# Optimization experiments

Hardware: AMD Instinct MI355X
Metric: run time of the kernel (lower is better)

## Reference

```python
import jax, jax.numpy as jnp
import numpy as np

B, L, A = 256, 512, 40          # proteins, residues per protein, atoms per drug
FD, FT, LD = 78, 54, 128        # drug feat, protein feat, latent dim
P = L + 1                       # residues + 1 appended drug super-node


def setup_inputs() -> dict:
    key = jax.random.key(0)
    ks = iter(jax.random.split(key, 48))
    Nd = B * A
    # drug graphs: chain bonds, both directions
    i = np.arange(A - 1)
    s = np.concatenate([i, i + 1]); d = np.concatenate([i + 1, i])
    off = (np.arange(B) * A)[:, None]
    drug_ei = jnp.asarray(np.stack([(s[None] + off).ravel(), (d[None] + off).ravel()]), jnp.int32)
    drug_batch = jnp.asarray(np.repeat(np.arange(B), A), jnp.int32)
    # protein graphs: residue chain + drug super-node (local idx L) connected to all residues in order
    r = np.arange(L - 1)
    ps = np.concatenate([r, r + 1, np.full(L, L), np.arange(L)])
    pd = np.concatenate([r + 1, r, np.arange(L), np.full(L, L)])
    poff = (np.arange(B) * P)[:, None]
    prot_ei = jnp.asarray(np.stack([(ps[None] + poff).ravel(), (pd[None] + poff).ravel()]), jnp.int32)
    prot_batch = jnp.asarray(np.repeat(np.arange(B), P), jnp.int32)
    E2 = B * (2 * (L - 1) + 2 * L)

    def lin(fi, fo):
        return jax.random.normal(next(ks), (fi, fo), jnp.float32) / np.float32(np.sqrt(fi))

    def vec(fo):
        return jnp.zeros((fo,), jnp.float32)

    return dict(
        drug_x=jax.random.normal(next(ks), (Nd, FD), jnp.float32),
        drug_ei=drug_ei, drug_batch=drug_batch,
        prot_x=jax.random.normal(next(ks), (B * P, FT), jnp.float32),
        prot_ei=prot_ei, prot_batch=prot_batch,
        prot_ea=jax.random.uniform(next(ks), (E2,), jnp.float32),
        W_c1d=lin(FD, FD), b_c1d=vec(FD),
        W_c2d=lin(FD, 2 * FD), b_c2d=vec(2 * FD),
        W_rd_g=lin(2 * FD, 2 * FD), b_rd_g=vec(2 * FD), W_rd_l=lin(2 * FD, 2 * FD),
        W_fg1d=lin(2 * FD, 1024), b_fg1d=vec(1024),
        W_fg2d=lin(1024, FT), b_fg2d=vec(FT),
        W_fg3d=lin(FT, 2 * LD), b_fg3d=vec(2 * LD),
        W_att1=lin(FT, FT), b_att1=vec(FT),
        W_att2=lin(FT, 1), b_att2=vec(1),
        W_c1t=lin(FT, LD), b_c1t=vec(LD),
        W_c2t=lin(LD, 2 * LD), b_c2t=vec(2 * LD),
        W_rt_g=lin(2 * LD, 2 * LD), b_rt_g=vec(2 * LD), W_rt_l=lin(2 * LD, 2 * LD),
        W_fg1t=lin(2 * LD, 1024), b_fg1t=vec(1024),
        W_fg2t=lin(1024, 2 * LD), b_fg2t=vec(2 * LD),
        W_fc1=lin(4 * LD, 1024), b_fc1=vec(1024),
        W_fc2=lin(1024, 512), b_fc2=vec(512),
        W_out=lin(512, 1), b_out=vec(1),
    )


def _gcn(x, W, b, src, dst, ew, n):
    # PyG GCNConv: symmetric norm with self-loops (fill value 1), optional edge weights
    h = x @ W
    deg = jax.ops.segment_sum(ew, dst, num_segments=n) + 1.0
    dinv = jax.lax.rsqrt(deg)
    norm = dinv[src] * ew * dinv[dst]
    agg = jax.ops.segment_sum(h[src] * norm[:, None], dst, num_segments=n)
    return agg + h * (dinv * dinv)[:, None] + b


def _rblock(x, Wg, bg, Wl, src, dst, ew, n):
    h = jax.nn.relu(_gcn(x, Wg, bg, src, dst, ew, n))
    return jax.nn.relu(h @ Wl + x)


def reference(drug_x, drug_ei, drug_batch, prot_x, prot_ei, prot_batch, prot_ea,
              W_c1d, b_c1d, W_c2d, b_c2d, W_rd_g, b_rd_g, W_rd_l,
              W_fg1d, b_fg1d, W_fg2d, b_fg2d, W_fg3d, b_fg3d,
              W_att1, b_att1, W_att2, b_att2,
              W_c1t, b_c1t, W_c2t, b_c2t, W_rt_g, b_rt_g, W_rt_l,
              W_fg1t, b_fg1t, W_fg2t, b_fg2t,
              W_fc1, b_fc1, W_fc2, b_fc2, W_out, b_out):
    relu = jax.nn.relu
    Nd, N2 = drug_x.shape[0], prot_x.shape[0]
    sd, dd = drug_ei[0], drug_ei[1]
    ewd = jnp.ones(sd.shape[0], drug_x.dtype)
    x = relu(_gcn(drug_x, W_c1d, b_c1d, sd, dd, ewd, Nd))
    x = relu(_gcn(x, W_c2d, b_c2d, sd, dd, ewd, Nd))
    for _ in range(4):  # shared-weight residual block applied num_rblock times
        x = _rblock(x, W_rd_g, b_rd_g, W_rd_l, sd, dd, ewd, Nd)
    xg = jax.ops.segment_max(x, drug_batch, num_segments=B)  # global max pool
    x = relu(xg @ W_fg1d + b_fg1d)
    x = x @ W_fg2d + b_fg2d                                   # [B, FT]
    x_chg = relu(x @ W_fg3d + b_fg3d)                          # [B, 2*LD]
    # vectorized per-protein attention (replaces the python loop over prot_lens)
    res = prot_x.reshape(B, P, FT)[:, :L]                      # residues only
    att = jnp.tanh(res @ W_att1 + b_att1) @ W_att2 + b_att2    # [B, L, 1]
    att = jax.nn.softmax(att[..., 0], axis=1)                  # [B, L]
    att_node = jnp.concatenate([att, jnp.zeros((B, 1), att.dtype)], 1).reshape(-1)
    drug_idx = (jnp.arange(B) + 1) * P - 1
    is_drug = jnp.zeros((N2,), bool).at[drug_idx].set(True)
    st, dt = prot_ei[0], prot_ei[1]
    # edges touching a drug super-node get that residue's attention weight
    ea = jnp.where(is_drug[st], att_node[dt], jnp.where(is_drug[dt], att_node[st], prot_ea))
    x2 = prot_x.at[drug_idx].set(x)                            # inject drug embeddings
    x2 = relu(_gcn(x2, W_c1t, b_c1t, st, dt, ea, N2))
    x2 = relu(_gcn(x2, W_c2t, b_c2t, st, dt, ea, N2))
    ew1 = jnp.ones(st.shape[0], x2.dtype)
    for _ in range(4):
        x2 = _rblock(x2, W_rt_g, b_rt_g, W_rt_l, st, dt, ew1, N2)
    x2r = x2.reshape(B, P, 2 * LD)
    x2g = x2r[:, :L].max(axis=1)                               # gmp over residues (drug node masked out)
    drug_after = x2r[:, L]
    x2v = relu(x2g @ W_fg1t + b_fg1t) @ W_fg2t + b_fg2t
    xm = jnp.maximum(drug_after, x_chg)                        # max_pool1d(kernel=2) over the pair
    xc = jnp.concatenate([xm, x2v], 1)
    xc = relu(xc @ W_fc1 + b_fc1)
    xc = relu(xc @ W_fc2 + b_fc2)
    return xc @ W_out + b_out
```

## Files before the change

kernel.cpp:

```cpp
#include <hip/hip_runtime.h>
#include <cstdio>

#define B_   256
#define L_   512
#define A_   40
#define FD_  78
#define FT_  54
#define LD_  128
#define P_   513
#define ND_  (B_*A_)
#define N2_  (B_*P_)
#define EB_  2046

typedef __attribute__((ext_vector_type(8))) short short8;
typedef __attribute__((ext_vector_type(4))) float floatx4;
typedef unsigned short u16;

__device__ __forceinline__ short f2bf(float f) {
    union { float f; unsigned u; } v; v.f = f;
    unsigned u = v.u;
    u += 0x7fff + ((u >> 16) & 1);
    return (short)(u >> 16);
}
__device__ __forceinline__ float bf2f(u16 s) {
    union { unsigned u; float f; } v; v.u = ((unsigned)s) << 16; return v.f;
}

#define TBK 32
#define LDK 40

__global__ __launch_bounds__(256) void gemm_mfma_k(
    const float* __restrict__ A, const short* __restrict__ WT,
    float* __restrict__ C, int M, int N, int K, int Kp)
{
    __shared__ short As[128 * LDK];
    __shared__ short Bs[128 * LDK];
    const int bm = blockIdx.y * 128;
    const int bn = blockIdx.x * 128;
    const int tid  = threadIdx.x;
    const int wave = tid >> 6, lane = tid & 63;
    const int wm = (wave >> 1) * 64, wn = (wave & 1) * 64;
    const int lrow = lane & 15, quad = lane >> 4;

    floatx4 acc[4][4] = {};

    for (int k0 = 0; k0 < Kp; k0 += TBK) {
#pragma unroll
        for (int it = 0; it < 2; ++it) {
            int g   = it * 256 + tid;
            int row = g >> 2, kg = g & 3;
            int kb  = k0 + kg * 8;
            const float* arow = A + (size_t)(bm + row) * K + kb;
            short8 av;
#pragma unroll
            for (int j = 0; j < 8; ++j) av[j] = (kb + j < K) ? f2bf(arow[j]) : (short)0;
            *(short8*)&As[row * LDK + kg * 8] = av;
            *(short8*)&Bs[row * LDK + kg * 8] = *(const short8*)(WT + (size_t)(bn + row) * Kp + kb);
        }
        __syncthreads();
        short8 af[4], bfv[4];
#pragma unroll
        for (int i = 0; i < 4; ++i)
            af[i] = *(short8*)&As[(wm + i * 16 + lrow) * LDK + quad * 8];
#pragma unroll
        for (int j = 0; j < 4; ++j)
            bfv[j] = *(short8*)&Bs[(wn + j * 16 + lrow) * LDK + quad * 8];
#pragma unroll
        for (int i = 0; i < 4; ++i)
#pragma unroll
            for (int j = 0; j < 4; ++j)
                acc[i][j] = __builtin_amdgcn_mfma_f32_16x16x32_bf16(af[i], bfv[j], acc[i][j], 0, 0, 0);
        __syncthreads();
    }
#pragma unroll
    for (int i = 0; i < 4; ++i) {
        int grow0 = bm + wm + i * 16 + quad * 4;
#pragma unroll
        for (int j = 0; j < 4; ++j) {
            int col = bn + wn + j * 16 + lrow;
            size_t base = (size_t)grow0 * N + col;
#pragma unroll
            for (int r = 0; r < 4; ++r)
                C[base + (size_t)r * N] = acc[i][j][r];
        }
    }
}

__global__ __launch_bounds__(256) void gemm_bb_k(
    const u16* __restrict__ A, int lda, const short* __restrict__ WT, int Kp,
    const u16* __restrict__ resid, u16* __restrict__ C, int N, int act)
{
    __shared__ short As[128 * LDK];
    __shared__ short Bs[128 * LDK];
    const int bm = blockIdx.y * 128;
    const int bn = blockIdx.x * 128;
    const int tid  = threadIdx.x;
    const int wave = tid >> 6, lane = tid & 63;
    const int wm = (wave >> 1) * 64, wn = (wave & 1) * 64;
    const int lrow = lane & 15, quad = lane >> 4;

    floatx4 acc[4][4] = {};

    for (int k0 = 0; k0 < Kp; k0 += TBK) {
#pragma unroll
        for (int it = 0; it < 2; ++it) {
            int g   = it * 256 + tid;
            int row = g >> 2, kg = g & 3;
            int kb  = k0 + kg * 8;
            *(short8*)&As[row * LDK + kg * 8] = *(const short8*)(A + (size_t)(bm + row) * lda + kb);
            *(short8*)&Bs[row * LDK + kg * 8] = *(const short8*)(WT + (size_t)(bn + row) * Kp + kb);
        }
        __syncthreads();
        short8 af[4], bfv[4];
#pragma unroll
        for (int i = 0; i < 4; ++i)
            af[i] = *(short8*)&As[(wm + i * 16 + lrow) * LDK + quad * 8];
#pragma unroll
        for (int j = 0; j < 4; ++j)
            bfv[j] = *(short8*)&Bs[(wn + j * 16 + lrow) * LDK + quad * 8];
#pragma unroll
        for (int i = 0; i < 4; ++i)
#pragma unroll
            for (int j = 0; j < 4; ++j)
                acc[i][j] = __builtin_amdgcn_mfma_f32_16x16x32_bf16(af[i], bfv[j], acc[i][j], 0, 0, 0);
        __syncthreads();
    }
#pragma unroll
    for (int i = 0; i < 4; ++i) {
        int grow0 = bm + wm + i * 16 + quad * 4;
#pragma unroll
        for (int j = 0; j < 4; ++j) {
            int col = bn + wn + j * 16 + lrow;
            size_t base = (size_t)grow0 * N + col;
#pragma unroll
            for (int r = 0; r < 4; ++r) {
                float v = acc[i][j][r];
                size_t idx = base + (size_t)r * N;
                if (resid) v += bf2f(resid[idx]);
                if (act)   v = fmaxf(v, 0.f);
                C[idx] = (u16)f2bf(v);
            }
        }
    }
}

template<int KT>
__global__ __launch_bounds__(256, 3) void gemm_n256pw_k(
    const u16* __restrict__ A, const short* __restrict__ WT,
    const u16* __restrict__ resid, u16* __restrict__ C, int act,
    const float* __restrict__ cInF, float* __restrict__ Wacc)
{
    constexpr int K = KT * TBK;
    __shared__ short As[64 * LDK];
    __shared__ short Bs[256 * LDK];
    const int bm = blockIdx.x * 64;
    const int tid  = threadIdx.x;
    const int wave = tid >> 6, lane = tid & 63;
    const int wn = wave * 64;
    const int lrow = lane & 15, quad = lane >> 4;
    const int srow = tid >> 2, skg = tid & 3;

    floatx4 acc[4][4] = {};

    short8 aR[KT];
#pragma unroll
    for (int kt = 0; kt < KT; ++kt)
        aR[kt] = *(const short8*)(A + (size_t)(bm + srow) * K + kt * TBK + skg * 8);
    short8 bReg[4];
#pragma unroll
    for (int it = 0; it < 4; ++it)
        bReg[it] = *(const short8*)(WT + (size_t)(it * 64 + srow) * K + skg * 8);

#pragma unroll
    for (int kt = 0; kt < KT; ++kt) {
        *(short8*)&As[srow * LDK + skg * 8] = aR[kt];
#pragma unroll
        for (int it = 0; it < 4; ++it)
            *(short8*)&Bs[(it * 64 + srow) * LDK + skg * 8] = bReg[it];
        __syncthreads();
        if (kt + 1 < KT) {
            int kn = (kt + 1) * TBK;
#pragma unroll
            for (int it = 0; it < 4; ++it)
                bReg[it] = *(const short8*)(WT + (size_t)(it * 64 + srow) * K + kn + skg * 8);
        }
        short8 af[4], bfv[4];
#pragma unroll
        for (int i = 0; i < 4; ++i)
            af[i] = *(short8*)&As[(i * 16 + lrow) * LDK + quad * 8];
#pragma unroll
        for (int j = 0; j < 4; ++j)
            bfv[j] = *(short8*)&Bs[(wn + j * 16 + lrow) * LDK + quad * 8];
#pragma unroll
        for (int i = 0; i < 4; ++i)
#pragma unroll
            for (int j = 0; j < 4; ++j)
                acc[i][j] = __builtin_amdgcn_mfma_f32_16x16x32_bf16(af[i], bfv[j], acc[i][j], 0, 0, 0);
        __syncthreads();
    }
#pragma unroll
    for (int i = 0; i < 4; ++i) {
        int grow0 = bm + i * 16 + quad * 4;
#pragma unroll
        for (int j = 0; j < 4; ++j) {
            int col = wn + j * 16 + lrow;
            size_t base = (size_t)grow0 * 256 + col;
#pragma unroll
            for (int r = 0; r < 4; ++r) {
                float v = acc[i][j][r];
                size_t idx = base + (size_t)r * 256;
                if (resid) v += bf2f(resid[idx]);
                if (act)   v = fmaxf(v, 0.f);
                C[idx] = (u16)f2bf(v);
            }
        }
    }
    if (cInF) {
        const int b0 = bm / P_;
        const int b1 = (bm + 63) / P_;
        float s0[4] = {0.f, 0.f, 0.f, 0.f};
        float s1[4] = {0.f, 0.f, 0.f, 0.f};
#pragma unroll
        for (int i = 0; i < 4; ++i) {
#pragma unroll
            for (int r = 0; r < 4; ++r) {
                int grow = bm + i * 16 + quad * 4 + r;
                float ci = cInF[grow];
                bool hi = (grow / P_) != b0;
#pragma unroll
                for (int j = 0; j < 4; ++j) {
                    float v = ci * acc[i][j][r];
                    if (hi) s1[j] += v; else s0[j] += v;
                }
            }
        }
#pragma unroll
        for (int j = 0; j < 4; ++j) {
            s0[j] += __shfl_xor(s0[j], 16);
            s0[j] += __shfl_xor(s0[j], 32);
            s1[j] += __shfl_xor(s1[j], 16);
            s1[j] += __shfl_xor(s1[j], 32);
        }
        if (quad == 0) {
#pragma unroll
            for (int j = 0; j < 4; ++j) {
                int col = wn + j * 16 + lrow;
                atomicAdd(&Wacc[(size_t)b0 * 256 + col], s0[j]);
                if (b1 != b0) atomicAdd(&Wacc[(size_t)b1 * 256 + col], s1[j]);
            }
        }
    }
}

template<int KT>
__global__ __launch_bounds__(256, 3) void gemm_aggl_k(
    const u16* __restrict__ U, const short* __restrict__ WT,
    const float* __restrict__ cPc, const float* __restrict__ cNc,
    const float* __restrict__ cDc, const float* __restrict__ cSc,
    const float* __restrict__ Wacc, const float* __restrict__ bias,
    const u16* __restrict__ resid, u16* __restrict__ C)
{
    constexpr int K = KT * TBK;
    __shared__ short As[64 * LDK];
    __shared__ short Bs[256 * LDK];
    const int bm = blockIdx.x * 64;
    const int tid  = threadIdx.x;
    const int wave = tid >> 6, lane = tid & 63;
    const int wn = wave * 64;
    const int lrow = lane & 15, quad = lane >> 4;
    const int srow = tid >> 2, skg = tid & 3;

    const int r    = bm + srow;
    const int bl   = r / P_;
    const int irow = r - bl * P_;
    const bool isD = (irow == L_);
    const size_t rD = (size_t)bl * P_ + L_;
    const int rm = (r == 0) ? 0 : r - 1;
    const int rp = (r == N2_ - 1) ? r : r + 1;
    const float cs = cSc[r];
    const float cp = isD ? 0.f : cPc[r];
    const float cn = isD ? 0.f : cNc[r];
    const float cd = isD ? 0.f : cDc[r];
    const float* wrow = Wacc + (size_t)bl * 256;

    floatx4 acc[4][4] = {};

    const u16* uSp = U + (size_t)r  * K + skg * 8;
    const u16* uMp = U + (size_t)rm * K + skg * 8;
    const u16* uPp = U + (size_t)rp * K + skg * 8;
    const u16* uDp = U + (size_t)rD * K + skg * 8;

    short8 uS[KT];
#pragma unroll
    for (int kt = 0; kt < KT; ++kt) uS[kt] = *(const short8*)(uSp + kt * TBK);
    short8 uM = *(const short8*)uMp;
    short8 uP = *(const short8*)uPp;
    short8 uD = *(const short8*)uDp;
    short8 bReg[4];
#pragma unroll
    for (int it = 0; it < 4; ++it)
        bReg[it] = *(const short8*)(WT + (size_t)(it * 64 + srow) * K + skg * 8);

#pragma unroll
    for (int kt = 0; kt < KT; ++kt) {
        const int kb = kt * TBK + skg * 8;
        float4 bi0 = *(const float4*)(bias + kb);
        float4 bi1 = *(const float4*)(bias + kb + 4);
        float bv[8] = {bi0.x, bi0.y, bi0.z, bi0.w, bi1.x, bi1.y, bi1.z, bi1.w};
        if (isD) {
            float4 w0 = *(const float4*)(wrow + kb);
            float4 w1 = *(const float4*)(wrow + kb + 4);
            bv[0] += w0.x; bv[1] += w0.y; bv[2] += w0.z; bv[3] += w0.w;
            bv[4] += w1.x; bv[5] += w1.y; bv[6] += w1.z; bv[7] += w1.w;
        }
        short8 av;
#pragma unroll
        for (int e = 0; e < 8; ++e) {
            float v = cs * bf2f((u16)uS[kt][e]) + cp * bf2f((u16)uM[e])
                    + cn * bf2f((u16)uP[e]) + cd * bf2f((u16)uD[e]) + bv[e];
            av[e] = f2bf(fmaxf(v, 0.f));
        }
        *(short8*)&As[srow * LDK + skg * 8] = av;
#pragma unroll
        for (int it = 0; it < 4; ++it)
            *(short8*)&Bs[(it * 64 + srow) * LDK + skg * 8] = bReg[it];
        __syncthreads();
        if (kt + 1 < KT) {
            const int kn = (kt + 1) * TBK;
            uM = *(const short8*)(uMp + kn);
            uP = *(const short8*)(uPp + kn);
            uD = *(const short8*)(uDp + kn);
#pragma unroll
            for (int it = 0; it < 4; ++it)
                bReg[it] = *(const short8*)(WT + (size_t)(it * 64 + srow) * K + kn + skg * 8);
        }
        short8 af[4], bfv[4];
#pragma unroll
        for (int i = 0; i < 4; ++i)
            af[i] = *(short8*)&As[(i * 16 + lrow) * LDK + quad * 8];
#pragma unroll
        for (int j = 0; j < 4; ++j)
            bfv[j] = *(short8*)&Bs[(wn + j * 16 + lrow) * LDK + quad * 8];
#pragma unroll
        for (int i = 0; i < 4; ++i)
#pragma unroll
            for (int j = 0; j < 4; ++j)
                acc[i][j] = __builtin_amdgcn_mfma_f32_16x16x32_bf16(af[i], bfv[j], acc[i][j], 0, 0, 0);
        __syncthreads();
    }
#pragma unroll
    for (int i = 0; i < 4; ++i) {
        int grow0 = bm + i * 16 + quad * 4;
#pragma unroll
        for (int j = 0; j < 4; ++j) {
            int col = wn + j * 16 + lrow;
            size_t base = (size_t)grow0 * 256 + col;
#pragma unroll
            for (int r2 = 0; r2 < 4; ++r2) {
                float v = acc[i][j][r2];
                size_t idx = base + (size_t)r2 * 256;
                v += bf2f(resid[idx]);
                v = fmaxf(v, 0.f);
                C[idx] = (u16)f2bf(v);
            }
        }
    }
}

static inline void gemm_n256(const u16* A, int K, const short* WT,
                             const u16* resid, u16* C, int act,
                             const float* cInF, float* Wacc, hipStream_t s)
{
    dim3 g(N2_ / 64), b(256);
    if (K == 128)
        hipLaunchKernelGGL((gemm_n256pw_k<4>), g, b, 0, s, A, WT, resid, C, act, cInF, Wacc);
    else
        hipLaunchKernelGGL((gemm_n256pw_k<8>), g, b, 0, s, A, WT, resid, C, act, cInF, Wacc);
}

__global__ void wt_cvt_k(const float* __restrict__ W, short* __restrict__ WT,
                         int K, int Nreal, int Kp, int Ntot)
{
    int idx = blockIdx.x * 256 + threadIdx.x;
    if (idx >= Ntot * Kp) return;
    int n = idx / Kp, k = idx - n * Kp;
    WT[idx] = (k < K && n < Nreal) ? f2bf(W[(size_t)k * Nreal + n]) : (short)0;
}

#define BM 64
#define BN 64
#define BKK 16
__global__ __launch_bounds__(256) void gemm_k(
    const float* __restrict__ Amat, const float* __restrict__ Wmat,
    const float* __restrict__ bias, const float* __restrict__ resid,
    float* __restrict__ Cmat, int M, int N, int K, int act)
{
    __shared__ float As[BKK][BM + 4];
    __shared__ float Ws[BKK][BN];
    const int bm = blockIdx.y * BM;
    const int bn = blockIdx.x * BN;
    const int tx = threadIdx.x, ty = threadIdx.y;
    const int tid = ty * 16 + tx;
    float acc[4][4] = {};

    for (int k0 = 0; k0 < K; k0 += BKK) {
#pragma unroll
        for (int j = 0; j < 4; ++j) {
            int l = tid + 256 * j;
            int m = l >> 4, kk = l & 15;
            int gm = bm + m, gk = k0 + kk;
            As[kk][m] = (gm < M && gk < K) ? Amat[(size_t)gm * K + gk] : 0.f;
        }
#pragma unroll
        for (int j = 0; j < 4; ++j) {
            int l = tid + 256 * j;
            int kk = l >> 6, n = l & 63;
            int gk = k0 + kk, gn = bn + n;
            Ws[kk][n] = (gk < K && gn < N) ? Wmat[(size_t)gk * N + gn] : 0.f;
        }
        __syncthreads();
#pragma unroll
        for (int k = 0; k < BKK; ++k) {
            float4 a4 = *(const float4*)&As[k][ty * 4];
            float4 w4 = *(const float4*)&Ws[k][tx * 4];
            float av[4] = {a4.x, a4.y, a4.z, a4.w};
            float wv[4] = {w4.x, w4.y, w4.z, w4.w};
#pragma unroll
            for (int i = 0; i < 4; ++i)
#pragma unroll
                for (int j = 0; j < 4; ++j)
                    acc[i][j] = fmaf(av[i], wv[j], acc[i][j]);
        }
        __syncthreads();
    }
#pragma unroll
    for (int i = 0; i < 4; ++i) {
        int gm = bm + ty * 4 + i;
        if (gm >= M) continue;
#pragma unroll
        for (int j = 0; j < 4; ++j) {
            int gn = bn + tx * 4 + j;
            if (gn >= N) continue;
            float v = acc[i][j];
            if (bias)  v += bias[gn];
            if (resid) v += resid[(size_t)gm * N + gn];
            if (act)   v = fmaxf(v, 0.f);
            Cmat[(size_t)gm * N + gn] = v;
        }
    }
}

static inline void gemm(const float* A, const float* W, const float* bias,
                        const float* resid, float* C, int M, int N, int K, int act,
                        hipStream_t s)
{
    dim3 g((N + BN - 1) / BN, (M + BM - 1) / BM), b(16, 16);
    hipLaunchKernelGGL(gemm_k, g, b, 0, s, A, W, bias, resid, C, M, N, K, act);
}

__global__ __launch_bounds__(256) void gemm_skA_k(
    const float* __restrict__ Amat, const float* __restrict__ Wmat,
    float* __restrict__ part, int M, int N, int K, int Kc)
{
    __shared__ float As[BKK][BM + 4];
    __shared__ float Ws[BKK][BN];
    const int bm = blockIdx.y * BM;
    const int bn = blockIdx.x * BN;
    const int sk = blockIdx.z;
    const int kb0  = sk * Kc;
    const int kend = min(K, kb0 + Kc);
    const int tx = threadIdx.x, ty = threadIdx.y;
    const int tid = ty * 16 + tx;
    float acc[4][4] = {};

    for (int k0 = kb0; k0 < kend; k0 += BKK) {
#pragma unroll
        for (int j = 0; j < 4; ++j) {
            int l = tid + 256 * j;
            int m = l >> 4, kk = l & 15;
            int gm = bm + m, gk = k0 + kk;
            As[kk][m] = (gm < M && gk < kend) ? Amat[(size_t)gm * K + gk] : 0.f;
        }
#pragma unroll
        for (int j = 0; j < 4; ++j) {
            int l = tid + 256 * j;
            int kk = l >> 6, n = l & 63;
            int gk = k0 + kk, gn = bn + n;
            Ws[kk][n] = (gk < kend && gn < N) ? Wmat[(size_t)gk * N + gn] : 0.f;
        }
        __syncthreads();
#pragma unroll
        for (int k = 0; k < BKK; ++k) {
            float4 a4 = *(const float4*)&As[k][ty * 4];
            float4 w4 = *(const float4*)&Ws[k][tx * 4];
            float av[4] = {a4.x, a4.y, a4.z, a4.w};
            float wv[4] = {w4.x, w4.y, w4.z, w4.w};
#pragma unroll
            for (int i = 0; i < 4; ++i)
#pragma unroll
                for (int j = 0; j < 4; ++j)
                    acc[i][j] = fmaf(av[i], wv[j], acc[i][j]);
        }
        __syncthreads();
    }
#pragma unroll
    for (int i = 0; i < 4; ++i) {
        int gm = bm + ty * 4 + i;
        if (gm >= M) continue;
#pragma unroll
        for (int j = 0; j < 4; ++j) {
            int gn = bn + tx * 4 + j;
            if (gn >= N) continue;
            part[((size_t)sk * M + gm) * N + gn] = acc[i][j];
        }
    }
}

__global__ void gemm_skB_k(const float* __restrict__ part, const float* __restrict__ bias,
                           float* __restrict__ C, int M, int N, int SK, int act)
{
    int idx = blockIdx.x * 256 + threadIdx.x;
    if (idx >= M * N) return;
    int n = idx % N;
    float v = bias ? bias[n] : 0.f;
    for (int s = 0; s < SK; ++s) v += part[(size_t)s * M * N + idx];
    if (act) v = fmaxf(v, 0.f);
    C[idx] = v;
}

static inline void gemm_sk(const float* A, const float* W, const float* bias,
                           float* C, float* skbuf, int M, int N, int K, int SK, int act,
                           hipStream_t s)
{
    int Kc = (K + SK - 1) / SK;
    dim3 g((N + 63) / 64, (M + 63) / 64, SK), b(16, 16);
    hipLaunchKernelGGL(gemm_skA_k, g, b, 0, s, A, W, skbuf, M, N, K, Kc);
    hipLaunchKernelGGL(gemm_skB_k, dim3((M * N + 255) / 256), dim3(256), 0, s,
                       skbuf, bias, C, M, N, SK, act);
}

__global__ void drug_agg_k(const float* __restrict__ h, const float* __restrict__ bias,
                           float* __restrict__ out, int F)
{
    int r = blockIdx.x;
    int a = r % A_;
    int t = threadIdx.x;
    if (t >= F) return;
    const float DI2 = 0.70710678118654752f;
    const float DI3 = 0.57735026918962576f;
    float da = (a == 0 || a == A_ - 1) ? DI2 : DI3;
    const float* hs = h + (size_t)r * F;
    float v = da * da * hs[t] + bias[t];
    if (a > 0) {
        float dp = (a - 1 == 0) ? DI2 : DI3;
        v += dp * da * hs[t - F];
    }
    if (a < A_ - 1) {
        float dn = (a + 1 == A_ - 1) ? DI2 : DI3;
        v += dn * da * hs[t + F];
    }
    out[(size_t)r * F + t] = fmaxf(v, 0.f);
}

__global__ void drug_max_k(const float* __restrict__ x, float* __restrict__ xg)
{
    int b = blockIdx.x, t = threadIdx.x;
    if (t >= 2 * FD_) return;
    const float* xb = x + (size_t)b * A_ * (2 * FD_);
    float m = -INFINITY;
    for (int a = 0; a < A_; ++a) m = fmaxf(m, xb[a * (2 * FD_) + t]);
    xg[b * (2 * FD_) + t] = m;
}

__global__ __launch_bounds__(256) void att_dot_k(
    const float* __restrict__ Hs, const float* __restrict__ b1,
    const float* __restrict__ W2, const float* __restrict__ b2,
    float* __restrict__ scores)
{
    int w = threadIdx.x >> 6, lane = threadIdx.x & 63;
    float b1v = (lane < FT_) ? b1[lane] : 0.f;
    float w2v = (lane < FT_) ? W2[lane] : 0.f;
    float b2v = b2[0];
    int base = blockIdx.x * 64 + w * 16;
    for (int rr = 0; rr < 16; ++rr) {
        int r = base + rr;
        float v = 0.f;
        if (lane < FT_) v = tanhf(Hs[(size_t)r * 128 + lane] + b1v) * w2v;
#pragma unroll
        for (int o = 32; o; o >>= 1) v += __shfl_down(v, o);
        if (lane == 0) {
            int bl = r / P_, i = r - bl * P_;
            if (i < L_) scores[bl * L_ + i] = v + b2v;
        }
    }
}

__global__ __launch_bounds__(512) void softmax_k(
    const float* __restrict__ scores, float* __restrict__ att, float* __restrict__ attsum)
{
    int b = blockIdx.x, t = threadIdx.x;
    __shared__ float sm[8];
    __shared__ float bcast;
    float v = scores[b * L_ + t];
    float m = v;
#pragma unroll
    for (int o = 32; o; o >>= 1) m = fmaxf(m, __shfl_down(m, o));
    if ((t & 63) == 0) sm[t >> 6] = m;
    __syncthreads();
    if (t == 0) { float mm = sm[0]; for (int i = 1; i < 8; ++i) mm = fmaxf(mm, sm[i]); bcast = mm; }
    __syncthreads();
    float mx = bcast;
    float e = expf(v - mx);
    float s = e;
#pragma unroll
    for (int o = 32; o; o >>= 1) s += __shfl_down(s, o);
    __syncthreads();
    if ((t & 63) == 0) sm[t >> 6] = s;
    __syncthreads();
    if (t == 0) { float ss = 0; for (int i = 0; i < 8; ++i) ss += sm[i]; bcast = ss; }
    __syncthreads();
    float a = e / bcast;
    att[b * L_ + t] = a;
    float s2 = a;
#pragma unroll
    for (int o = 32; o; o >>= 1) s2 += __shfl_down(s2, o);
    __syncthreads();
    if ((t & 63) == 0) sm[t >> 6] = s2;
    __syncthreads();
    if (t == 0) { float ss = 0; for (int i = 0; i < 8; ++i) ss += sm[i]; attsum[b] = ss; }
}

__global__ void coef_deg_k(const float* __restrict__ prot_ea, const float* __restrict__ att,
                           const float* __restrict__ attsum, float* __restrict__ dinv, int use_ea)
{
    int r = blockIdx.x * 256 + threadIdx.x;
    if (r >= N2_) return;
    int b = r / P_, i = r - b * P_;
    float deg;
    if (i == L_) {
        deg = 1.f + (use_ea ? attsum[b] : (float)L_);
    } else {
        float wP = (i >= 1)      ? (use_ea ? prot_ea[b * EB_ + (i - 1)]   : 1.f) : 0.f;
        float wN = (i <= L_ - 2) ? (use_ea ? prot_ea[b * EB_ + 511 + i]   : 1.f) : 0.f;
        float wD = use_ea ? att[b * L_ + i] : 1.f;
        deg = 1.f + wP + wN + wD;
    }
    dinv[r] = rsqrtf(deg);
}

__global__ void coef_k(const float* __restrict__ dinv, const float* __restrict__ prot_ea,
                       const float* __restrict__ att, float* __restrict__ cP, float* __restrict__ cN,
                       float* __restrict__ cD, float* __restrict__ cS, float* __restrict__ cIn,
                       float* __restrict__ cInF, int use_ea)
{
    int r = blockIdx.x * 256 + threadIdx.x;
    if (r >= N2_) return;
    int b = r / P_, i = r - b * P_;
    float di = dinv[r];
    cS[r] = di * di;
    if (i == L_) { cP[r] = 0.f; cN[r] = 0.f; cD[r] = 0.f; cInF[r] = 0.f; return; }
    float wP = (i >= 1)      ? (use_ea ? prot_ea[b * EB_ + (i - 1)] : 1.f) : 0.f;
    float wN = (i <= L_ - 2) ? (use_ea ? prot_ea[b * EB_ + 511 + i] : 1.f) : 0.f;
    float wD = use_ea ? att[b * L_ + i] : 1.f;
    float dD = dinv[b * P_ + L_];
    cP[r] = (i >= 1)      ? dinv[r - 1] * wP * di : 0.f;
    cN[r] = (i <= L_ - 2) ? dinv[r + 1] * wN * di : 0.f;
    cD[r] = dD * wD * di;
    float ci = di * wD * dD;
    cIn[b * L_ + i] = ci;
    cInF[r] = ci;
}

template<int F>
__global__ __launch_bounds__(256) void prot_agg_res_k(
    const u16* __restrict__ h, const float* __restrict__ cP,
    const float* __restrict__ cN, const float* __restrict__ cD,
    const float* __restrict__ cS, const float* __restrict__ cIn,
    const float* __restrict__ bias, u16* __restrict__ outp,
    float* __restrict__ Wacc)
{
    constexpr int G = F / 8;
    constexpr int RPB = 256 / G;
    __shared__ float pacc[RPB * F];
    int t = threadIdx.x;
    int rl = t / G, g = t - rl * G;
    int base = blockIdx.x * RPB;
    int r = base + rl;
    int bl = r / P_, i = r - bl * P_;
    int f0 = g * 8;
    const u16* hs = h + (size_t)r * F + f0;
    if (i == L_) {
#pragma unroll
        for (int e = 0; e < 8; ++e) pacc[rl * F + f0 + e] = 0.f;
    } else {
        const u16* hd = h + ((size_t)bl * P_ + L_) * F + f0;
        float cs = cS[r], cd = cD[r], cp = cP[r], cn = cN[r];
        float ci = cIn[bl * L_ + i];
        short8 vs = *(const short8*)hs;
        short8 vd = *(const short8*)hd;
        short8 vp = *(const short8*)(hs - (i > 0 ? F : 0));
        short8 vn = *(const short8*)(hs + F);
        short8 ov;
#pragma unroll
        for (int e = 0; e < 8; ++e) {
            float hv = bf2f((u16)vs[e]);
            pacc[rl * F + f0 + e] = ci * hv;
            float v = cs * hv + cd * bf2f((u16)vd[e]) + bias[f0 + e];
            v += cp * bf2f((u16)vp[e]);
            v += cn * bf2f((u16)vn[e]);
            ov[e] = f2bf(fmaxf(v, 0.f));
        }
        *(short8*)(outp + (size_t)r * F + f0) = ov;
    }
    __syncthreads();
    int f = t;
    if (f < F) {
        int b0   = base / P_;
        int bend = (base + RPB - 1) / P_;
        float s0 = 0.f, s1 = 0.f;
#pragma unroll
        for (int rr = 0; rr < RPB; ++rr) {
            float v = pacc[rr * F + f];
            if ((base + rr) / P_ == b0) s0 += v; else s1 += v;
        }
        atomicAdd(&Wacc[(size_t)b0 * F + f], s0);
        if (bend != b0) atomicAdd(&Wacc[(size_t)bend * F + f], s1);
    }
}

__global__ void drug_fin_k(const float* __restrict__ Wacc, const u16* __restrict__ h,
                           const float* __restrict__ cS, const float* __restrict__ bias,
                           u16* __restrict__ outp, int F)
{
    int bl = blockIdx.x, t = threadIdx.x;
    if (t >= F) return;
    size_t rD = (size_t)bl * P_ + L_;
    float v = Wacc[(size_t)bl * F + t] + cS[rD] * bf2f(h[rD * F + t]) + bias[t];
    outp[rD * F + t] = (u16)f2bf(fmaxf(v, 0.f));
}

__global__ void xin_k(const float* __restrict__ prot_x, const float* __restrict__ t2d,
                      u16* __restrict__ Xin)
{
    int idx = blockIdx.x * 256 + threadIdx.x;
    if (idx >= N2_ * 64) return;
    int r = idx >> 6, t = idx & 63;
    int bl = r / P_, i = r - bl * P_;
    float v = 0.f;
    if (t < FT_) v = (i == L_) ? t2d[bl * FT_ + t] : prot_x[(size_t)r * FT_ + t];
    Xin[idx] = (u16)f2bf(v);
}

__global__ __launch_bounds__(256) void x2g_bf2_k(const u16* __restrict__ X,
                                                 float* __restrict__ x2g, float* __restrict__ da)
{
    __shared__ float red[2048];
    int t = threadIdx.x;
    int rl = t >> 5, g = t & 31;
    int bl = blockIdx.x, f0 = g * 8;
    const u16* xb = X + (size_t)bl * P_ * 256;
    float m[8];
#pragma unroll
    for (int e = 0; e < 8; ++e) m[e] = -INFINITY;
    for (int j = rl; j < L_; j += 8) {
        short8 v = *(const short8*)(xb + (size_t)j * 256 + f0);
#pragma unroll
        for (int e = 0; e < 8; ++e) m[e] = fmaxf(m[e], bf2f((u16)v[e]));
    }
#pragma unroll
    for (int e = 0; e < 8; ++e) red[rl * 256 + f0 + e] = m[e];
    __syncthreads();
    if (rl == 0) {
        short8 vd = *(const short8*)(xb + (size_t)L_ * 256 + f0);
#pragma unroll
        for (int e = 0; e < 8; ++e) {
            float v = red[f0 + e];
            for (int rr = 1; rr < 8; ++rr) v = fmaxf(v, red[rr * 256 + f0 + e]);
            x2g[bl * 256 + f0 + e] = v;
            da[bl * 256 + f0 + e] = bf2f((u16)vd[e]);
        }
    }
}

__global__ void build_xc_k(const float* __restrict__ da, const float* __restrict__ x_chg,
                           const float* __restrict__ x2v, float* __restrict__ xc)
{
    int idx = blockIdx.x * 256 + threadIdx.x;
    if (idx >= B_ * 512) return;
    int b = idx >> 9, c = idx & 511;
    float v = (c < 256) ? fmaxf(da[b * 256 + c], x_chg[b * 256 + c])
                        : x2v[b * 256 + (c - 256)];
    xc[idx] = v;
}

__global__ __launch_bounds__(64) void out_k(const float* __restrict__ f2,
                                            const float* __restrict__ W,
                                            const float* __restrict__ bias,
                                            float* __restrict__ out)
{
    int row = blockIdx.x, t = threadIdx.x;
    float v = 0.f;
    for (int k = t; k < 512; k += 64) v = fmaf(f2[(size_t)row * 512 + k], W[k], v);
#pragma unroll
    for (int o = 32; o; o >>= 1) v += __shfl_down(v, o);
    if (t == 0) out[row] = v + bias[0];
}

extern "C" void kernel_launch(void* const* d_in, const int* in_sizes, int n_in,
                              void* d_out, int out_size, void* d_ws, size_t ws_size,
                              hipStream_t stream)
{
    const float* drug_x  = (const float*)d_in[0];
    const float* prot_x  = (const float*)d_in[3];
    const float* prot_ea = (const float*)d_in[6];
    const float* W_c1d = (const float*)d_in[7];   const float* b_c1d = (const float*)d_in[8];
    const float* W_c2d = (const float*)d_in[9];   const float* b_c2d = (const float*)d_in[10];
    const float* W_rd_g = (const float*)d_in[11]; const float* b_rd_g = (const float*)d_in[12];
    const float* W_rd_l = (const float*)d_in[13];
    const float* W_fg1d = (const float*)d_in[14]; const float* b_fg1d = (const float*)d_in[15];
    const float* W_fg2d = (const float*)d_in[16]; const float* b_fg2d = (const float*)d_in[17];
    const float* W_fg3d = (const float*)d_in[18]; const float* b_fg3d = (const float*)d_in[19];
    const float* W_att1 = (const float*)d_in[20]; const float* b_att1 = (const float*)d_in[21];
    const float* W_att2 = (const float*)d_in[22]; const float* b_att2 = (const float*)d_in[23];
    const float* W_c1t = (const float*)d_in[24];  const float* b_c1t = (const float*)d_in[25];
    const float* W_c2t = (const float*)d_in[26];  const float* b_c2t = (const float*)d_in[27];
    const float* W_rt_g = (const float*)d_in[28]; const float* b_rt_g = (const float*)d_in[29];
    const float* W_rt_l = (const float*)d_in[30];
    const float* W_fg1t = (const float*)d_in[31]; const float* b_fg1t = (const float*)d_in[32];
    const float* W_fg2t = (const float*)d_in[33]; const float* b_fg2t = (const float*)d_in[34];
    const float* W_fc1 = (const float*)d_in[35];  const float* b_fc1 = (const float*)d_in[36];
    const float* W_fc2 = (const float*)d_in[37];  const float* b_fc2 = (const float*)d_in[38];
    const float* W_out = (const float*)d_in[39];  const float* b_out = (const float*)d_in[40];
    float* out = (float*)d_out;

    float* ws = (float*)d_ws;
    size_t off = 0;
    auto alloc = [&](size_t n) {
        n = (n + 3) & ~(size_t)3;
        float* p = ws + off; off += n; return p;
    };

    u16* U = (u16*)alloc((size_t)N2_ * 128);
    u16* V = (u16*)alloc((size_t)N2_ * 128);
    u16* X = (u16*)alloc((size_t)N2_ * 128);
    u16* Xin = (u16*)alloc((size_t)N2_ * 32);
    float* Hs = (float*)U;
    float* Wacc = alloc(B_ * 256);
    float* dA = alloc((size_t)ND_ * 156);
    float* dB = alloc((size_t)ND_ * 156);
    float* dC = alloc((size_t)ND_ * 156);
    float* xg    = alloc(B_ * 156);
    float* t1d   = alloc(B_ * 1024);
    float* t2d   = alloc(B_ * FT_);
    float* x_chg = alloc(B_ * 256);
    float* scores = alloc(B_ * 512);
    float* att    = alloc(B_ * 512);
    float* attsum = alloc(B_);
    float* dinvE = alloc(N2_);
    float* cPE = alloc(N2_); float* cNE = alloc(N2_); float* cDE = alloc(N2_); float* cSE = alloc(N2_);
    float* cInE = alloc(B_ * 512);
    float* cInFE = alloc(N2_);
    float* dinvO = alloc(N2_);
    float* cPO = alloc(N2_); float* cNO = alloc(N2_); float* cDO = alloc(N2_); float* cSO = alloc(N2_);
    float* cInO = alloc(B_ * 512);
    float* cInFO = alloc(N2_);
    float* x2g = alloc(B_ * 256);
    float* dafter = alloc(B_ * 256);
    float* t1t = alloc(B_ * 1024);
    float* x2v = alloc(B_ * 256);
    float* xc  = alloc(B_ * 512);
    float* f1  = alloc(B_ * 1024);
    float* f2  = alloc(B_ * 512);
    float* skbuf = alloc((size_t)2 * 1024 * 1024);
    short* WT_c1t = (short*)alloc(128 * 64 / 2);
    short* WT_c2t = (short*)alloc(256 * 128 / 2);
    short* WT_rtg = (short*)alloc(256 * 256 / 2);
    short* WT_rtl = (short*)alloc(256 * 256 / 2);
    short* WT_att = (short*)alloc(128 * 64 / 2);

    if (off * sizeof(float) > ws_size) {
        fprintf(stderr, "kernel_launch: workspace too small: need %zu, have %zu\n",
                off * sizeof(float), ws_size);
        return;
    }

    hipLaunchKernelGGL(wt_cvt_k, dim3((128 * 64 + 255) / 256), dim3(256), 0, stream,  W_c1t, WT_c1t, FT_, 128, 64, 128);
    hipLaunchKernelGGL(wt_cvt_k, dim3((256 * 128 + 255) / 256), dim3(256), 0, stream, W_c2t, WT_c2t, 128, 256, 128, 256);
    hipLaunchKernelGGL(wt_cvt_k, dim3((256 * 256 + 255) / 256), dim3(256), 0, stream, W_rt_g, WT_rtg, 256, 256, 256, 256);
    hipLaunchKernelGGL(wt_cvt_k, dim3((256 * 256 + 255) / 256), dim3(256), 0, stream, W_rt_l, WT_rtl, 256, 256, 256, 256);
    hipLaunchKernelGGL(wt_cvt_k, dim3((128 * 64 + 255) / 256), dim3(256), 0, stream,  W_att1, WT_att, FT_, FT_, 64, 128);

    gemm(drug_x, W_c1d, nullptr, nullptr, dB, ND_, FD_, FD_, 0, stream);
    hipLaunchKernelGGL(drug_agg_k, dim3(ND_), dim3(128), 0, stream, dB, b_c1d, dA, FD_);
    gemm(dA, W_c2d, nullptr, nullptr, dB, ND_, 2 * FD_, FD_, 0, stream);
    hipLaunchKernelGGL(drug_agg_k, dim3(ND_), dim3(192), 0, stream, dB, b_c2d, dA, 2 * FD_);
    for (int it = 0; it < 4; ++it) {
        gemm(dA, W_rd_g, nullptr, nullptr, dB, ND_, 2 * FD_, 2 * FD_, 0, stream);
        hipLaunchKernelGGL(drug_agg_k, dim3(ND_), dim3(192), 0, stream, dB, b_rd_g, dC, 2 * FD_);
        gemm(dC, W_rd_l, nullptr, dA, dB, ND_, 2 * FD_, 2 * FD_, 1, stream);
        float* tmp = dA; dA = dB; dB = tmp;
    }
    hipLaunchKernelGGL(drug_max_k, dim3(B_), dim3(192), 0, stream, dA, xg);
    gemm_sk(xg,  W_fg1d, b_fg1d, t1d,   skbuf, B_, 1024, 156, 4, 1, stream);
    gemm_sk(t1d, W_fg2d, b_fg2d, t2d,   skbuf, B_, FT_, 1024, 16, 0, stream);
    gemm_sk(t2d, W_fg3d, b_fg3d, x_chg, skbuf, B_, 2 * LD_, FT_, 2, 1, stream);

    {
        dim3 g(1, N2_ / 128), b(256);
        hipLaunchKernelGGL(gemm_mfma_k, g, b, 0, stream, prot_x, WT_att, Hs, N2_, 128, FT_, 64);
    }
    hipLaunchKernelGGL(att_dot_k, dim3(N2_ / 64), dim3(256), 0, stream, Hs, b_att1, W_att2, b_att2, scores);
    hipLaunchKernelGGL(softmax_k, dim3(B_), dim3(512), 0, stream, scores, att, attsum);

    hipLaunchKernelGGL(coef_deg_k, dim3((N2_ + 255) / 256), dim3(256), 0, stream, prot_ea, att, attsum, dinvE, 1);
    hipLaunchKernelGGL(coef_k, dim3((N2_ + 255) / 256), dim3(256), 0, stream, dinvE, prot_ea, att, cPE, cNE, cDE, cSE, cInE, cInFE, 1);
    hipLaunchKernelGGL(coef_deg_k, dim3((N2_ + 255) / 256), dim3(256), 0, stream, prot_ea, att, attsum, dinvO, 0);
    hipLaunchKernelGGL(coef_k, dim3((N2_ + 255) / 256), dim3(256), 0, stream, dinvO, prot_ea, att, cPO, cNO, cDO, cSO, cInO, cInFO, 0);

    hipLaunchKernelGGL(xin_k, dim3((N2_ * 64 + 255) / 256), dim3(256), 0, stream, prot_x, t2d, Xin);

    {
        dim3 g(1, N2_ / 128), b(256);
        hipLaunchKernelGGL(gemm_bb_k, g, b, 0, stream, Xin, 64, WT_c1t, 64,
                           (const u16*)nullptr, U, 128, 0);
    }
    hipMemsetAsync(Wacc, 0, B_ * 128 * sizeof(float), stream);
    hipLaunchKernelGGL((prot_agg_res_k<128>), dim3(N2_ / 16), dim3(256), 0, stream,
                       U, cPE, cNE, cDE, cSE, cInE, b_c1t, V, Wacc);
    hipLaunchKernelGGL(drug_fin_k, dim3(B_), dim3(128), 0, stream, Wacc, U, cSE, b_c1t, V, 128);
    gemm_n256(V, 128, WT_c2t, (const u16*)nullptr, U, 0, nullptr, nullptr, stream);
    hipMemsetAsync(Wacc, 0, B_ * 256 * sizeof(float), stream);
    hipLaunchKernelGGL((prot_agg_res_k<256>), dim3(N2_ / 8), dim3(256), 0, stream,
                       U, cPE, cNE, cDE, cSE, cInE, b_c2t, X, Wacc);
    hipLaunchKernelGGL(drug_fin_k, dim3(B_), dim3(256), 0, stream, Wacc, U, cSE, b_c2t, X, 256);

    for (int it = 0; it < 4; ++it) {
        hipMemsetAsync(Wacc, 0, B_ * 256 * sizeof(float), stream);
        gemm_n256(X, 256, WT_rtg, (const u16*)nullptr, U, 0, cInFO, Wacc, stream);
        {
            dim3 g(N2_ / 64), b(256);
            hipLaunchKernelGGL((gemm_aggl_k<8>), g, b, 0, stream,
                               U, WT_rtl, cPO, cNO, cDO, cSO, Wacc, b_rt_g, X, X);
        }
    }

    hipLaunchKernelGGL(x2g_bf2_k, dim3(B_), dim3(256), 0, stream, X, x2g, dafter);

    gemm_sk(x2g, W_fg1t, b_fg1t, t1t, skbuf, B_, 1024, 256, 8, 1, stream);
    gemm_sk(t1t, W_fg2t, b_fg2t, x2v, skbuf, B_, 256, 1024, 16, 0, stream);
    hipLaunchKernelGGL(build_xc_k, dim3(B_ * 512 / 256), dim3(256), 0, stream, dafter, x_chg, x2v, xc);
    gemm_sk(xc, W_fc1, b_fc1, f1, skbuf, B_, 1024, 512, 8, 1, stream);
    gemm_sk(f1, W_fc2, b_fc2, f2, skbuf, B_, 512, 1024, 16, 1, stream);
    hipLaunchKernelGGL(out_k, dim3(B_), dim3(64), 0, stream, f2, W_out, b_out, out);
}
```

Before: 1.281 ms.

## Fuse residual block's two GEMMs into one kernel with halo rows in LDS

The separate global-transform GEMM and the aggregate-plus-local GEMM are merged into one kernel. Each block computes U for its 64 rows plus 8 halo rows on each side, keeps U in LDS, and then does the chain aggregation and the second GEMM without writing U to global memory. Drug super-node rows are handled by two small per-graph kernels (udrug_k and drug_row_k), and X is ping-ponged between buffers. This removes a full N2x256 global round trip per iteration. In exchange it adds redundant halo compute, larger LDS use that lowers occupancy to 2 blocks, and two extra launches per iteration.

```diff
diff --git a/kernel.cpp b/kernel.cpp
--- a/kernel.cpp
+++ b/kernel.cpp
@@ -28,6 +28,7 @@
 
 #define TBK 32
 #define LDK 40
+#define UBS 264
 
 __global__ __launch_bounds__(256) void gemm_mfma_k(
     const float* __restrict__ A, const short* __restrict__ WT,
@@ -252,121 +253,6 @@
     }
 }
 
-template<int KT>
-__global__ __launch_bounds__(256, 3) void gemm_aggl_k(
-    const u16* __restrict__ U, const short* __restrict__ WT,
-    const float* __restrict__ cPc, const float* __restrict__ cNc,
-    const float* __restrict__ cDc, const float* __restrict__ cSc,
-    const float* __restrict__ Wacc, const float* __restrict__ bias,
-    const u16* __restrict__ resid, u16* __restrict__ C)
-{
-    constexpr int K = KT * TBK;
-    __shared__ short As[64 * LDK];
-    __shared__ short Bs[256 * LDK];
-    const int bm = blockIdx.x * 64;
-    const int tid  = threadIdx.x;
-    const int wave = tid >> 6, lane = tid & 63;
-    const int wn = wave * 64;
-    const int lrow = lane & 15, quad = lane >> 4;
-    const int srow = tid >> 2, skg = tid & 3;
-
-    const int r    = bm + srow;
-    const int bl   = r / P_;
-    const int irow = r - bl * P_;
-    const bool isD = (irow == L_);
-    const size_t rD = (size_t)bl * P_ + L_;
-    const int rm = (r == 0) ? 0 : r - 1;
-    const int rp = (r == N2_ - 1) ? r : r + 1;
-    const float cs = cSc[r];
-    const float cp = isD ? 0.f : cPc[r];
-    const float cn = isD ? 0.f : cNc[r];
-    const float cd = isD ? 0.f : cDc[r];
-    const float* wrow = Wacc + (size_t)bl * 256;
-
-    floatx4 acc[4][4] = {};
-
-    const u16* uSp = U + (size_t)r  * K + skg * 8;
-    const u16* uMp = U + (size_t)rm * K + skg * 8;
-    const u16* uPp = U + (size_t)rp * K + skg * 8;
-    const u16* uDp = U + (size_t)rD * K + skg * 8;
-
-    short8 uS[KT];
-#pragma unroll
-    for (int kt = 0; kt < KT; ++kt) uS[kt] = *(const short8*)(uSp + kt * TBK);
-    short8 uM = *(const short8*)uMp;
-    short8 uP = *(const short8*)uPp;
-    short8 uD = *(const short8*)uDp;
-    short8 bReg[4];
-#pragma unroll
-    for (int it = 0; it < 4; ++it)
-        bReg[it] = *(const short8*)(WT + (size_t)(it * 64 + srow) * K + skg * 8);
-
-#pragma unroll
-    for (int kt = 0; kt < KT; ++kt) {
-        const int kb = kt * TBK + skg * 8;
-        float4 bi0 = *(const float4*)(bias + kb);
-        float4 bi1 = *(const float4*)(bias + kb + 4);
-        float bv[8] = {bi0.x, bi0.y, bi0.z, bi0.w, bi1.x, bi1.y, bi1.z, bi1.w};
-        if (isD) {
-            float4 w0 = *(const float4*)(wrow + kb);
-            float4 w1 = *(const float4*)(wrow + kb + 4);
-            bv[0] += w0.x; bv[1] += w0.y; bv[2] += w0.z; bv[3] += w0.w;
-            bv[4] += w1.x; bv[5] += w1.y; bv[6] += w1.z; bv[7] += w1.w;
-        }
-        short8 av;
-#pragma unroll
-        for (int e = 0; e < 8; ++e) {
-            float v = cs * bf2f((u16)uS[kt][e]) + cp * bf2f((u16)uM[e])
-                    + cn * bf2f((u16)uP[e]) + cd * bf2f((u16)uD[e]) + bv[e];
-            av[e] = f2bf(fmaxf(v, 0.f));
-        }
-        *(short8*)&As[srow * LDK + skg * 8] = av;
-#pragma unroll
-        for (int it = 0; it < 4; ++it)
-            *(short8*)&Bs[(it * 64 + srow) * LDK + skg * 8] = bReg[it];
-        __syncthreads();
-        if (kt + 1 < KT) {
-            const int kn = (kt + 1) * TBK;
-            uM = *(const short8*)(uMp + kn);
-            uP = *(const short8*)(uPp + kn);
-            uD = *(const short8*)(uDp + kn);
-#pragma unroll
-            for (int it = 0; it < 4; ++it)
-                bReg[it] = *(const short8*)(WT + (size_t)(it * 64 + srow) * K + kn + skg * 8);
-        }
-        short8 af[4], bfv[4];
-#pragma unroll
-        for (int i = 0; i < 4; ++i)
-            af[i] = *(short8*)&As[(i * 16 + lrow) * LDK + quad * 8];
-#pragma unroll
-        for (int j = 0; j < 4; ++j)
-            bfv[j] = *(short8*)&Bs[(wn + j * 16 + lrow) * LDK + quad * 8];
-#pragma unroll
-        for (int i = 0; i < 4; ++i)
-#pragma unroll
-            for (int j = 0; j < 4; ++j)
-                acc[i][j] = __builtin_amdgcn_mfma_f32_16x16x32_bf16(af[i], bfv[j], acc[i][j], 0, 0, 0);
-        __syncthreads();
-    }
-#pragma unroll
-    for (int i = 0; i < 4; ++i) {
-        int grow0 = bm + i * 16 + quad * 4;
-#pragma unroll
-        for (int j = 0; j < 4; ++j) {
-            int col = wn + j * 16 + lrow;
-            size_t base = (size_t)grow0 * 256 + col;
-#pragma unroll
-            for (int r2 = 0; r2 < 4; ++r2) {
-                float v = acc[i][j][r2];
-                size_t idx = base + (size_t)r2 * 256;
-                v += bf2f(resid[idx]);
-                v = fmaxf(v, 0.f);
-                C[idx] = (u16)f2bf(v);
-            }
-        }
-    }
-}
-
 static inline void gemm_n256(const u16* A, int K, const short* WT,
                              const u16* resid, u16* C, int act,
                              const float* cInF, float* Wacc, hipStream_t s)
@@ -376,6 +262,248 @@
         hipLaunchKernelGGL((gemm_n256pw_k<4>), g, b, 0, s, A, WT, resid, C, act, cInF, Wacc);
     else
         hipLaunchKernelGGL((gemm_n256pw_k<8>), g, b, 0, s, A, WT, resid, C, act, cInF, Wacc);
+}
+
+template<int KT>
+__global__ __launch_bounds__(256, 2) void fused_res_k(
+    const u16* __restrict__ X, const short* __restrict__ WTg,
+    const short* __restrict__ WTl, const u16* __restrict__ Udrug,
+    const float* __restrict__ cPc, const float* __restrict__ cNc,
+    const float* __restrict__ cDc, const float* __restrict__ cSc,
+    const float* __restrict__ cInF, const float* __restrict__ bias_g,
+    float* __restrict__ Wacc, u16* __restrict__ Xn)
+{
+    constexpr int K = KT * TBK;
+    __shared__ short Ub[80 * UBS];
+    __shared__ short As[80 * LDK];
+    const int bm    = blockIdx.x * 64;
+    const int gbase = bm - 8;
+    const int tid   = threadIdx.x;
+    const int wave  = tid >> 6, lane = tid & 63;
+    const int wn    = wave * 64;
+    const int lrow  = lane & 15, quad = lane >> 4;
+    const int srow  = tid >> 2, skg = tid & 3;
+
+    int g1 = gbase + srow;
+    g1 = g1 < 0 ? 0 : g1;
+    const u16* ap1 = X + (size_t)g1 * K + skg * 8;
+    int g2 = gbase + 64 + srow;
+    g2 = g2 >= N2_ ? N2_ - 1 : g2;
+    const u16* ap2 = X + (size_t)g2 * K + skg * 8;
+    const bool w0 = (wave == 0);
+
+    const short* bgp0 = WTg + (size_t)(wn +  0 + lrow) * K + quad * 8;
+    const short* bgp1 = WTg + (size_t)(wn + 16 + lrow) * K + quad * 8;
+    const short* bgp2 = WTg + (size_t)(wn + 32 + lrow) * K + quad * 8;
+    const short* bgp3 = WTg + (size_t)(wn + 48 + lrow) * K + quad * 8;
+
+    floatx4 acc[5][4] = {};
+    short8 aP1[2], aP2[2], bP[2][4];
+    aP1[0] = *(const short8*)ap1;
+    if (w0) aP2[0] = *(const short8*)ap2;
+    bP[0][0] = *(const short8*)bgp0;
+    bP[0][1] = *(const short8*)bgp1;
+    bP[0][2] = *(const short8*)bgp2;
+    bP[0][3] = *(const short8*)bgp3;
+
+#pragma unroll
+    for (int kt = 0; kt < KT; ++kt) {
+        const int cur = kt & 1, nxt = cur ^ 1;
+        *(short8*)&As[srow * LDK + skg * 8] = aP1[cur];
+        if (w0) *(short8*)&As[(64 + srow) * LDK + skg * 8] = aP2[cur];
+        __syncthreads();
+        if (kt + 1 < KT) {
+            const int kn = (kt + 1) * TBK;
+            aP1[nxt] = *(const short8*)(ap1 + kn);
+            if (w0) aP2[nxt] = *(const short8*)(ap2 + kn);
+            bP[nxt][0] = *(const short8*)(bgp0 + kn);
+            bP[nxt][1] = *(const short8*)(bgp1 + kn);
+            bP[nxt][2] = *(const short8*)(bgp2 + kn);
+            bP[nxt][3] = *(const short8*)(bgp3 + kn);
+        }
+        short8 af[5];
+#pragma unroll
+        for (int i = 0; i < 5; ++i)
+            af[i] = *(short8*)&As[(i * 16 + lrow) * LDK + quad * 8];
+#pragma unroll
+        for (int i = 0; i < 5; ++i)
+#pragma unroll
+            for (int j = 0; j < 4; ++j)
+                acc[i][j] = __builtin_amdgcn_mfma_f32_16x16x32_bf16(af[i], bP[cur][j], acc[i][j], 0, 0, 0);
+        __syncthreads();
+    }
+
+    {
+        const int b0 = bm / P_;
+        const int b1 = (bm + 63) / P_;
+        float s0[4] = {0.f, 0.f, 0.f, 0.f};
+        float s1[4] = {0.f, 0.f, 0.f, 0.f};
+#pragma unroll
+        for (int i = 0; i < 5; ++i) {
+#pragma unroll
+            for (int r = 0; r < 4; ++r) {
+                int wr = i * 16 + quad * 4 + r;
+                if (wr >= 8 && wr < 72) {
+                    int grow = gbase + wr;
+                    float ci = cInF[grow];
+                    bool hi = (grow / P_) != b0;
+#pragma unroll
+                    for (int j = 0; j < 4; ++j) {
+                        float v = ci * acc[i][j][r];
+                        if (hi) s1[j] += v; else s0[j] += v;
+                    }
+                }
+            }
+        }
+#pragma unroll
+        for (int j = 0; j < 4; ++j) {
+            s0[j] += __shfl_xor(s0[j], 16);
+            s0[j] += __shfl_xor(s0[j], 32);
+            s1[j] += __shfl_xor(s1[j], 16);
+            s1[j] += __shfl_xor(s1[j], 32);
+        }
+        if (quad == 0) {
+#pragma unroll
+            for (int j = 0; j < 4; ++j) {
+                int col = wn + j * 16 + lrow;
+                atomicAdd(&Wacc[(size_t)b0 * 256 + col], s0[j]);
+                if (b1 != b0) atomicAdd(&Wacc[(size_t)b1 * 256 + col], s1[j]);
+            }
+        }
+    }
+
+#pragma unroll
+    for (int i = 0; i < 5; ++i)
+#pragma unroll
+        for (int r = 0; r < 4; ++r) {
+            int wr = i * 16 + quad * 4 + r;
+#pragma unroll
+            for (int j = 0; j < 4; ++j)
+                Ub[wr * UBS + wn + j * 16 + lrow] = f2bf(acc[i][j][r]);
+        }
+    __syncthreads();
+
+    const int r    = bm + srow;
+    const int bl   = r / P_;
+    const int irow = r - bl * P_;
+    const bool isD = (irow == L_);
+    const float cs = isD ? 0.f : cSc[r];
+    const float cp = isD ? 0.f : cPc[r];
+    const float cn = isD ? 0.f : cNc[r];
+    const float cd = isD ? 0.f : cDc[r];
+    const u16* udp = Udrug + (size_t)bl * 256;
+
+    const short* blp0 = WTl + (size_t)(wn +  0 + lrow) * K + quad * 8;
+    const short* blp1 = WTl + (size_t)(wn + 16 + lrow) * K + quad * 8;
+    const short* blp2 = WTl + (size_t)(wn + 32 + lrow) * K + quad * 8;
+    const short* blp3 = WTl + (size_t)(wn + 48 + lrow) * K + quad * 8;
+
+    floatx4 acc2[4][4] = {};
+    short8 bl2[2][4];
+    bl2[0][0] = *(const short8*)blp0;
+    bl2[0][1] = *(const short8*)blp1;
+    bl2[0][2] = *(const short8*)blp2;
+    bl2[0][3] = *(const short8*)blp3;
+
+#pragma unroll
+    for (int kt = 0; kt < KT; ++kt) {
+        const int cur = kt & 1, nxt = cur ^ 1;
+        const int c0 = kt * TBK + skg * 8;
+        short8 uS = *(short8*)&Ub[(8 + srow) * UBS + c0];
+        short8 uM = *(short8*)&Ub[(7 + srow) * UBS + c0];
+        short8 uP = *(short8*)&Ub[(9 + srow) * UBS + c0];
+        short8 ud = *(const short8*)(udp + c0);
+        float4 bi0 = *(const float4*)(bias_g + c0);
+        float4 bi1 = *(const float4*)(bias_g + c0 + 4);
+        float bv[8] = {bi0.x, bi0.y, bi0.z, bi0.w, bi1.x, bi1.y, bi1.z, bi1.w};
+        short8 av;
+#pragma unroll
+        for (int e = 0; e < 8; ++e) {
+            float v = cs * bf2f((u16)uS[e]) + cp * bf2f((u16)uM[e])
+                    + cn * bf2f((u16)uP[e]) + cd * bf2f((u16)ud[e]) + bv[e];
+            av[e] = f2bf(fmaxf(v, 0.f));
+        }
+        *(short8*)&As[srow * LDK + skg * 8] = av;
+        __syncthreads();
+        if (kt + 1 < KT) {
+            const int kn = (kt + 1) * TBK;
+            bl2[nxt][0] = *(const short8*)(blp0 + kn);
+            bl2[nxt][1] = *(const short8*)(blp1 + kn);
+            bl2[nxt][2] = *(const short8*)(blp2 + kn);
+            bl2[nxt][3] = *(const short8*)(blp3 + kn);
+        }
+        short8 af2[4];
+#pragma unroll
+        for (int i = 0; i < 4; ++i)
+            af2[i] = *(short8*)&As[(i * 16 + lrow) * LDK + quad * 8];
+#pragma unroll
+        for (int i = 0; i < 4; ++i)
+#pragma unroll
+            for (int j = 0; j < 4; ++j)
+                acc2[i][j] = __builtin_amdgcn_mfma_f32_16x16x32_bf16(af2[i], bl2[cur][j], acc2[i][j], 0, 0, 0);
+        __syncthreads();
+    }
+
+#pragma unroll
+    for (int i = 0; i < 4; ++i) {
+        int grow0 = bm + i * 16 + quad * 4;
+#pragma unroll
+        for (int j = 0; j < 4; ++j) {
+            int col = wn + j * 16 + lrow;
+            size_t base = (size_t)grow0 * 256 + col;
+#pragma unroll
+            for (int r2 = 0; r2 < 4; ++r2) {
+                float v = acc2[i][j][r2];
+                size_t idx = base + (size_t)r2 * 256;
+                v += bf2f(X[idx]);
+                v = fmaxf(v, 0.f);
+                Xn[idx] = (u16)f2bf(v);
+            }
+        }
+    }
+}
+
+__global__ __launch_bounds__(256) void udrug_k(
+    const u16* __restrict__ Xold, const short* __restrict__ WTg,
+    u16* __restrict__ Udrug)
+{
+    __shared__ float xr[256];
+    int b = blockIdx.x, t = threadIdx.x;
+    size_t rD = (size_t)b * P_ + L_;
+    xr[t] = bf2f(Xold[rD * 256 + t]);
+    __syncthreads();
+    const short* wrow = WTg + (size_t)t * 256;
+    float v = 0.f;
+    for (int k = 0; k < 256; k += 8) {
+        short8 w = *(const short8*)(wrow + k);
+#pragma unroll
+        for (int e = 0; e < 8; ++e) v += xr[k + e] * bf2f((u16)w[e]);
+    }
+    Udrug[(size_t)b * 256 + t] = (u16)f2bf(v);
+}
+
+__global__ __launch_bounds__(256) void drug_row_k(
+    const float* __restrict__ Wacc, const u16* __restrict__ Udrug,
+    const float* __restrict__ cSc, const float* __restrict__ bias_g,
+    const short* __restrict__ WTl, const u16* __restrict__ Xold,
+    u16* __restrict__ Xn)
+{
+    __shared__ float a2[256];
+    int b = blockIdx.x, t = threadIdx.x;
+    size_t rD = (size_t)b * P_ + L_;
+    float u = bf2f(Udrug[(size_t)b * 256 + t]);
+    float av = fmaxf(Wacc[(size_t)b * 256 + t] + cSc[rD] * u + bias_g[t], 0.f);
+    a2[t] = bf2f((u16)f2bf(av));
+    __syncthreads();
+    const short* wrow = WTl + (size_t)t * 256;
+    float v = 0.f;
+    for (int k = 0; k < 256; k += 8) {
+        short8 w = *(const short8*)(wrow + k);
+#pragma unroll
+        for (int e = 0; e < 8; ++e) v += a2[k + e] * bf2f((u16)w[e]);
+    }
+    v += bf2f(Xold[rD * 256 + t]);
+    Xn[rD * 256 + t] = (u16)f2bf(fmaxf(v, 0.f));
 }
 
 __global__ void wt_cvt_k(const float* __restrict__ W, short* __restrict__ WT,
@@ -846,6 +974,7 @@
     u16* Xin = (u16*)alloc((size_t)N2_ * 32);
     float* Hs = (float*)U;
     float* Wacc = alloc(B_ * 256);
+    u16* Udrug = (u16*)alloc(B_ * 128);
     float* dA = alloc((size_t)ND_ * 156);
     float* dB = alloc((size_t)ND_ * 156);
     float* dC = alloc((size_t)ND_ * 156);
@@ -934,17 +1063,20 @@
                        U, cPE, cNE, cDE, cSE, cInE, b_c2t, X, Wacc);
     hipLaunchKernelGGL(drug_fin_k, dim3(B_), dim3(256), 0, stream, Wacc, U, cSE, b_c2t, X, 256);
 
+    u16* Xc = X;
+    u16* Xo = U;
     for (int it = 0; it < 4; ++it) {
         hipMemsetAsync(Wacc, 0, B_ * 256 * sizeof(float), stream);
-        gemm_n256(X, 256, WT_rtg, (const u16*)nullptr, U, 0, cInFO, Wacc, stream);
-        {
-            dim3 g(N2_ / 64), b(256);
-            hipLaunchKernelGGL((gemm_aggl_k<8>), g, b, 0, stream,
-                               U, WT_rtl, cPO, cNO, cDO, cSO, Wacc, b_rt_g, X, X);
-        }
-    }
-
-    hipLaunchKernelGGL(x2g_bf2_k, dim3(B_), dim3(256), 0, stream, X, x2g, dafter);
+        hipLaunchKernelGGL(udrug_k, dim3(B_), dim3(256), 0, stream, Xc, WT_rtg, Udrug);
+        hipLaunchKernelGGL((fused_res_k<8>), dim3(N2_ / 64), dim3(256), 0, stream,
+                           Xc, WT_rtg, WT_rtl, Udrug,
+                           cPO, cNO, cDO, cSO, cInFO, b_rt_g, Wacc, Xo);
+        hipLaunchKernelGGL(drug_row_k, dim3(B_), dim3(256), 0, stream,
+                           Wacc, Udrug, cSO, b_rt_g, WT_rtl, Xc, Xo);
+        u16* t = Xc; Xc = Xo; Xo = t;
+    }
+
+    hipLaunchKernelGGL(x2g_bf2_k, dim3(B_), dim3(256), 0, stream, Xc, x2g, dafter);
 
     gemm_sk(x2g, W_fg1t, b_fg1t, t1t, skbuf, B_, 1024, 256, 8, 1, stream);
     gemm_sk(t1t, W_fg2t, b_fg2t, x2v, skbuf, B_, 256, 1024, 16, 0, stream);
```

Result: slower. 1.348 ms (+5.2%).
